# Optimization experiments

Hardware: AMD Instinct MI355X
Metric: run time of the kernel (lower is better)

## Reference

```python
import jax, jax.numpy as jnp
import numpy as np

D = 256      # input channels
DK = 64      # key/query/value channels
BS, W, H = 8, 64, 64


def setup_inputs() -> dict:
    key = jax.random.key(0)
    k1, k2, k3, k4 = jax.random.split(key, 4)
    v = jax.random.normal(k1, (BS, D, W, H), dtype=jnp.float32)
    # conv1x1 weights collapse to plain matrices over the channel dim
    Wqkv = jax.random.normal(k2, (3 * DK, D), dtype=jnp.float32) * 0.02
    Wout = jax.random.normal(k3, (D, DK), dtype=jnp.float32) * 0.02
    gamma = jax.random.normal(k4, (1,), dtype=jnp.float32)  # original inits to 0; nonzero for a non-degenerate baseline
    return {"v": v, "Wqkv": Wqkv, "Wout": Wout, "gamma": gamma}


def reference(v, Wqkv, Wout, gamma):
    bs, c, w, h = v.shape
    n = w * h
    d_k = Wout.shape[1]
    x = v.reshape(bs, c, n)                      # (b, c, n)
    qkv = jnp.einsum('oc,bcn->bon', Wqkv, x)      # 1x1 conv == channel matmul
    q = qkv[:, :d_k]                              # (b, dk, n)
    k = qkv[:, d_k:2 * d_k]
    val = qkv[:, 2 * d_k:]
    s = jnp.einsum('bdi,bdj->bij', q, k)          # (b, n, n) = query^T key
    beta = jax.nn.softmax(s, axis=2)              # exp(s - logsumexp(s, axis=2))
    y = jnp.einsum('bdi,bij->bdj', val, beta)     # bmm(value, beta)
    o = jnp.einsum('od,bdn->bon', Wout, y) * gamma[0] + x
    return o.reshape(bs, c, w, h)
```

## Files before the change

### kernel.cpp

```cpp
#include <hip/hip_runtime.h>

typedef unsigned short ushort_t;
typedef __bf16 bf16x8 __attribute__((ext_vector_type(8)));
typedef short short4v __attribute__((ext_vector_type(4)));
typedef float f32x4 __attribute__((ext_vector_type(4)));
typedef unsigned int uint4v __attribute__((ext_vector_type(4)));
typedef unsigned int uint2v __attribute__((ext_vector_type(2)));

#define NTOK 4096
#define DMODEL 256
#define DK 64
#define BS 8
#define LN2INV 1.44269504088896f

__device__ __forceinline__ ushort_t f2bf(float f) {
  unsigned u = __builtin_bit_cast(unsigned, f);
  u += 0x7fffu + ((u >> 16) & 1u);
  return (ushort_t)(u >> 16);
}
__device__ __forceinline__ float bf2f(ushort_t s) {
  return __builtin_bit_cast(float, ((unsigned)s) << 16);
}
__device__ __forceinline__ bf16x8 lds_frag(const ushort_t* p) {
  return __builtin_bit_cast(bf16x8, *(const uint4v*)p);
}
__device__ __forceinline__ float fexp2(float x) {
#if __has_builtin(__builtin_amdgcn_exp2f)
  return __builtin_amdgcn_exp2f(x);
#else
  return exp2f(x);
#endif
}
__device__ __forceinline__ unsigned bfpack(float x, float y) {
  return __builtin_amdgcn_perm(__builtin_bit_cast(unsigned, y),
                               __builtin_bit_cast(unsigned, x), 0x07060302u);
}
__device__ __forceinline__ f32x4 mfma16(short4v a, short4v b, f32x4 c) {
#if defined(__HIP_DEVICE_COMPILE__)
#if __has_builtin(__builtin_amdgcn_mfma_f32_16x16x16bf16_1k)
  return __builtin_amdgcn_mfma_f32_16x16x16bf16_1k(a, b, c, 0, 0, 0);
#else
  typedef __bf16 bf16x4 __attribute__((ext_vector_type(4)));
  return __builtin_amdgcn_mfma_f32_16x16x16_bf16(__builtin_bit_cast(bf16x4, a),
                                                 __builtin_bit_cast(bf16x4, b), c, 0, 0, 0);
#endif
#else
  (void)a; (void)b;
  return c;
#endif
}

__global__ __launch_bounds__(256) void k_convert(const float* __restrict__ Wqkv,
                                                 const float* __restrict__ Wout,
                                                 ushort_t* __restrict__ Wb,
                                                 ushort_t* __restrict__ Woutb) {
  int i = blockIdx.x * 256 + threadIdx.x;
  if (i < 3 * DK * DMODEL) {
    float w = Wqkv[i];
    if (i < DK * DMODEL) w *= LN2INV;
    Wb[i] = f2bf(w);
  } else {
    int j = i - 3 * DK * DMODEL;
    Woutb[j] = f2bf(Wout[j]);
  }
}

__global__ __launch_bounds__(256) void k_transpose(const float* __restrict__ x,
                                                   ushort_t* __restrict__ xT) {
  const int id = blockIdx.x;
  const int b = id & 7;
  const int rest = id >> 3;
  const int c0 = (rest & 3) * 64;
  const int n0 = (rest >> 2) * 64;
  const int tid = threadIdx.x;
  __shared__ __align__(16) ushort_t t[64 * 72];
  const float* xb = x + (size_t)b * DMODEL * NTOK;
  ushort_t* xTb = xT + (size_t)b * NTOK * DMODEL;
#pragma unroll
  for (int kr = 0; kr < 2; kr++) {
    int s = tid + 256 * kr;
    int c = s >> 3, ns = (s & 7) * 8;
    const float* src = xb + (size_t)(c0 + c) * NTOK + n0 + ns;
    f32x4 a = *(const f32x4*)src;
    f32x4 bq = *(const f32x4*)(src + 4);
    uint4v o;
    o.x = (unsigned)f2bf(a[0]) | ((unsigned)f2bf(a[1]) << 16);
    o.y = (unsigned)f2bf(a[2]) | ((unsigned)f2bf(a[3]) << 16);
    o.z = (unsigned)f2bf(bq[0]) | ((unsigned)f2bf(bq[1]) << 16);
    o.w = (unsigned)f2bf(bq[2]) | ((unsigned)f2bf(bq[3]) << 16);
    *(uint4v*)(t + c * 72 + ns) = o;
  }
  __syncthreads();
#pragma unroll
  for (int kr = 0; kr < 2; kr++) {
    int s = tid + 256 * kr;
    int n = s >> 3, cs = (s & 7) * 8;
    unsigned e0 = t[(cs + 0) * 72 + n], e1 = t[(cs + 1) * 72 + n];
    unsigned e2 = t[(cs + 2) * 72 + n], e3 = t[(cs + 3) * 72 + n];
    unsigned e4 = t[(cs + 4) * 72 + n], e5 = t[(cs + 5) * 72 + n];
    unsigned e6 = t[(cs + 6) * 72 + n], e7 = t[(cs + 7) * 72 + n];
    uint4v o;
    o.x = e0 | (e1 << 16); o.y = e2 | (e3 << 16);
    o.z = e4 | (e5 << 16); o.w = e6 | (e7 << 16);
    *(uint4v*)(xTb + (size_t)(n0 + n) * DMODEL + c0 + cs) = o;
  }
}

__global__ __launch_bounds__(256) void k_qkv(const ushort_t* __restrict__ xT,
                                             const ushort_t* __restrict__ W,
                                             ushort_t* __restrict__ QT,
                                             ushort_t* __restrict__ KT,
                                             ushort_t* __restrict__ Vv) {
  const int id = blockIdx.x;
  const int b = id & 7;
  const int n0 = (id >> 3) * 64;
  const int tid = threadIdx.x;
  const int lane = tid & 63, wv = tid >> 6;
  const int quad = lane >> 4, l15 = lane & 15;
  __shared__ __align__(16) ushort_t lw[192 * 40];
  __shared__ __align__(16) ushort_t lx[64 * 40];
  f32x4 acc[3][4];
  const f32x4 zero4 = {0.f, 0.f, 0.f, 0.f};
#pragma unroll
  for (int i = 0; i < 3; i++)
#pragma unroll
    for (int j = 0; j < 4; j++) acc[i][j] = zero4;

  const ushort_t* xTb = xT + ((size_t)b * NTOK + n0) * DMODEL;

  for (int c0 = 0; c0 < DMODEL; c0 += 32) {
    __syncthreads();
#pragma unroll
    for (int kr = 0; kr < 3; kr++) {
      int s = tid + 256 * kr;
      int o = s >> 2, cs = (s & 3) * 8;
      *(uint4v*)(lw + o * 40 + cs) = *(const uint4v*)(W + o * DMODEL + c0 + cs);
    }
    {
      int n = tid >> 2, cs = (tid & 3) * 8;
      *(uint4v*)(lx + n * 40 + cs) = *(const uint4v*)(xTb + (size_t)n * DMODEL + c0 + cs);
    }
    __syncthreads();
    bf16x8 bb[4];
#pragma unroll
    for (int nt = 0; nt < 4; nt++) bb[nt] = lds_frag(lx + (nt * 16 + l15) * 40 + quad * 8);
#pragma unroll
    for (int mt = 0; mt < 3; mt++) {
      bf16x8 a = lds_frag(lw + (wv * 48 + mt * 16 + l15) * 40 + quad * 8);
#pragma unroll
      for (int nt = 0; nt < 4; nt++)
        acc[mt][nt] = __builtin_amdgcn_mfma_f32_16x16x32_bf16(a, bb[nt], acc[mt][nt], 0, 0, 0);
    }
  }
#pragma unroll
  for (int mt = 0; mt < 3; mt++) {
    int o = wv * 48 + mt * 16 + quad * 4;
#pragma unroll
    for (int nt = 0; nt < 4; nt++) {
      int n = n0 + nt * 16 + l15;
      f32x4 v4 = acc[mt][nt];
      if (o < 128) {
        ushort_t* dst = (o < 64) ? (QT + ((size_t)b * NTOK + n) * DK + o)
                                 : (KT + ((size_t)b * NTOK + n) * DK + (o - 64));
        uint2v ww;
        ww.x = (unsigned)f2bf(v4[0]) | ((unsigned)f2bf(v4[1]) << 16);
        ww.y = (unsigned)f2bf(v4[2]) | ((unsigned)f2bf(v4[3]) << 16);
        *(uint2v*)dst = ww;
      } else {
        int d = o - 128;
#pragma unroll
        for (int r = 0; r < 4; r++)
          Vv[((size_t)b * DK + d + r) * NTOK + n] = f2bf(v4[r]);
      }
    }
  }
}

__global__ __launch_bounds__(256) void k_rsum(const ushort_t* __restrict__ QT,
                                              const ushort_t* __restrict__ KT,
                                              float* __restrict__ Rp) {
  const int id = blockIdx.x;
  const int b = id & 7;
  const int rest = id >> 3;
  const int i0 = (rest & 31) * 128;
  const int jh = rest >> 5;
  const int tid = threadIdx.x;
  const int lane = tid & 63, wv = tid >> 6;
  const int quad = lane >> 4, l15 = lane & 15;
  __shared__ __align__(16) ushort_t lq[128 * 72];
  __shared__ __align__(16) ushort_t lk[2][64 * 72];
  const ushort_t* QTb = QT + ((size_t)b * NTOK + i0) * DK;
  const ushort_t* KTb = KT + ((size_t)b * NTOK + jh * 2048) * DK;
#pragma unroll
  for (int kr = 0; kr < 4; kr++) {
    int s = tid + 256 * kr;
    int row = s >> 3, ds = (s & 7) * 8;
    *(uint4v*)(lq + row * 72 + ds) = *(const uint4v*)(QTb + (size_t)row * DK + ds);
  }
#pragma unroll
  for (int kr = 0; kr < 2; kr++) {
    int s = tid + 256 * kr;
    int row = s >> 3, ds = (s & 7) * 8;
    *(uint4v*)(lk[0] + row * 72 + ds) = *(const uint4v*)(KTb + (size_t)row * DK + ds);
  }
  __syncthreads();
  bf16x8 aa[2][2];
#pragma unroll
  for (int isub = 0; isub < 2; isub++) {
    aa[isub][0] = lds_frag(lq + (wv * 32 + isub * 16 + l15) * 72 + quad * 8);
    aa[isub][1] = lds_frag(lq + (wv * 32 + isub * 16 + l15) * 72 + 32 + quad * 8);
  }
  float lsum[2][4];
#pragma unroll
  for (int i = 0; i < 2; i++)
#pragma unroll
    for (int r = 0; r < 4; r++) lsum[i][r] = 0.f;
  const f32x4 zero4 = {0.f, 0.f, 0.f, 0.f};

  auto stage = [&](ushort_t* dstb, int itn) {
    const ushort_t* src = KTb + (size_t)itn * 64 * DK;
#pragma unroll
    for (int kr = 0; kr < 2; kr++) {
      int s = tid + 256 * kr;
      int row = s >> 3, ds = (s & 7) * 8;
      *(uint4v*)(dstb + row * 72 + ds) = *(const uint4v*)(src + (size_t)row * DK + ds);
    }
  };
  auto body = [&](const ushort_t* kb) {
#pragma unroll
    for (int nt = 0; nt < 4; nt++) {
      bf16x8 b0 = lds_frag(kb + (nt * 16 + l15) * 72 + quad * 8);
      bf16x8 b1 = lds_frag(kb + (nt * 16 + l15) * 72 + 32 + quad * 8);
#pragma unroll
      for (int isub = 0; isub < 2; isub++) {
        f32x4 s4 = __builtin_amdgcn_mfma_f32_16x16x32_bf16(aa[isub][0], b0, zero4, 0, 0, 0);
        s4 = __builtin_amdgcn_mfma_f32_16x16x32_bf16(aa[isub][1], b1, s4, 0, 0, 0);
        lsum[isub][0] += fexp2(s4[0]);
        lsum[isub][1] += fexp2(s4[1]);
        lsum[isub][2] += fexp2(s4[2]);
        lsum[isub][3] += fexp2(s4[3]);
      }
    }
  };

  for (int it2 = 0; it2 < 16; it2++) {
    int it = it2 * 2;
    stage(lk[1], it + 1);
    body(lk[0]);
    __syncthreads();
    if (it2 < 15) stage(lk[0], it + 2);
    body(lk[1]);
    __syncthreads();
  }

#pragma unroll
  for (int isub = 0; isub < 2; isub++)
#pragma unroll
    for (int r = 0; r < 4; r++)
#pragma unroll
      for (int off = 1; off < 16; off <<= 1) lsum[isub][r] += __shfl_xor(lsum[isub][r], off);
  if (l15 < 8) {
    int rr = l15 & 3, isub = l15 >> 2;
    float va = (rr == 0) ? lsum[0][0] : (rr == 1) ? lsum[0][1] : (rr == 2) ? lsum[0][2] : lsum[0][3];
    float vb = (rr == 0) ? lsum[1][0] : (rr == 1) ? lsum[1][1] : (rr == 2) ? lsum[1][2] : lsum[1][3];
    float v = isub ? vb : va;
    Rp[((size_t)(jh * 8 + b)) * NTOK + i0 + wv * 32 + isub * 16 + quad * 4 + rr] = v;
  }
}

__global__ __launch_bounds__(256) void k_rv(const float* __restrict__ Rp,
                                            ushort_t* __restrict__ Vv) {
  const int id = blockIdx.x;
  const int b = id & 7;
  const int ibase = (id >> 3) * 256;
  const int tid = threadIdx.x;
  __shared__ float lrr[256];
  size_t g = (size_t)b * NTOK + ibase + tid;
  lrr[tid] = 1.0f / (Rp[g] + Rp[(size_t)8 * NTOK + g]);
  __syncthreads();
  const int dsub = tid >> 5;
  const int ioff = (tid & 31) * 8;
#pragma unroll
  for (int d8 = 0; d8 < 8; d8++) {
    int d = d8 * 8 + dsub;
    ushort_t* vp = Vv + ((size_t)b * DK + d) * NTOK + ibase + ioff;
    uint4v v0 = *(const uint4v*)vp;
    uint4v o0;
    unsigned* vi = (unsigned*)&v0;
    unsigned* oo = (unsigned*)&o0;
#pragma unroll
    for (int w = 0; w < 4; w++) {
      float e0 = bf2f((ushort_t)(vi[w] & 0xffff)) * lrr[ioff + 2 * w];
      float e1 = bf2f((ushort_t)(vi[w] >> 16)) * lrr[ioff + 2 * w + 1];
      oo[w] = (unsigned)f2bf(e0) | ((unsigned)f2bf(e1) << 16);
    }
    *(uint4v*)vp = o0;
  }
}

__global__ __launch_bounds__(256) void k_pv(const ushort_t* __restrict__ QT,
                                            const ushort_t* __restrict__ KT,
                                            const ushort_t* __restrict__ Vv,
                                            ushort_t* __restrict__ Yp) {
  const int id = blockIdx.x;
  const int b = id & 7;
  const int rest = id >> 3;
  const int j0 = (rest & 63) * 64;
  const int ih = rest >> 6;
  const int tid = threadIdx.x;
  const int lane = tid & 63, wv = tid >> 6;
  const int quad = lane >> 4, l15 = lane & 15;

  __shared__ __align__(16) ushort_t pool[18432];
#define LQ(buf) (pool + (buf) * 4608)
#define LV(buf) (pool + 9216 + (buf) * 4608)
  float* rbuf = (float*)pool;
  ushort_t* pbuf = pool + 8704;

  const ushort_t* KTb = KT + ((size_t)b * NTOK + j0) * DK;
  const ushort_t* QTb = QT + ((size_t)b * NTOK + ih * 2048) * DK;
  const ushort_t* Vbb = Vv + (size_t)b * DK * NTOK + ih * 2048;

#pragma unroll
  for (int kr = 0; kr < 2; kr++) {
    int s = tid + 256 * kr;
    int row = s >> 3, ds = (s & 7) * 8;
    *(uint4v*)(LQ(0) + row * 72 + ds) = *(const uint4v*)(KTb + (size_t)row * DK + ds);
  }
  __syncthreads();
  bf16x8 kb0[4], kb1[4];
#pragma unroll
  for (int nt = 0; nt < 4; nt++) {
    kb0[nt] = lds_frag(LQ(0) + (nt * 16 + l15) * 72 + quad * 8);
    kb1[nt] = lds_frag(LQ(0) + (nt * 16 + l15) * 72 + 32 + quad * 8);
  }
  __syncthreads();
#pragma unroll
  for (int kr = 0; kr < 2; kr++) {
    int s = tid + 256 * kr;
    int row = s >> 3, ds = (s & 7) * 8;
    *(uint4v*)(LQ(0) + row * 72 + ds) = *(const uint4v*)(QTb + (size_t)row * DK + ds);
    *(uint4v*)(LV(0) + row * 72 + ds) = *(const uint4v*)(Vbb + (size_t)row * NTOK + ds);
  }
  __syncthreads();

  const f32x4 zero4 = {0.f, 0.f, 0.f, 0.f};
  f32x4 yt[4][4];
#pragma unroll
  for (int i = 0; i < 4; i++)
#pragma unroll
    for (int j = 0; j < 4; j++) yt[i][j] = zero4;

  auto stage = [&](ushort_t* lqn, ushort_t* lvn, int itn) {
    const ushort_t* qsrc = QTb + (size_t)itn * 64 * DK;
    const ushort_t* vsrc = Vbb + itn * 64;
#pragma unroll
    for (int kr = 0; kr < 2; kr++) {
      int s = tid + 256 * kr;
      int row = s >> 3, ds = (s & 7) * 8;
      *(uint4v*)(lqn + row * 72 + ds) = *(const uint4v*)(qsrc + (size_t)row * DK + ds);
      *(uint4v*)(lvn + row * 72 + ds) = *(const uint4v*)(vsrc + (size_t)row * NTOK + ds);
    }
  };
  auto body = [&](const ushort_t* lqc, const ushort_t* lvc) {
    bf16x8 a0 = lds_frag(lqc + (wv * 16 + l15) * 72 + quad * 8);
    bf16x8 a1 = lds_frag(lqc + (wv * 16 + l15) * 72 + 32 + quad * 8);
    short4v vf[4];
#pragma unroll
    for (int dsub = 0; dsub < 4; dsub++)
      vf[dsub] = __builtin_bit_cast(short4v,
          *(const uint2v*)(lvc + (dsub * 16 + l15) * 72 + wv * 16 + quad * 4));
#pragma unroll
    for (int nt = 0; nt < 4; nt++) {
      f32x4 s4 = __builtin_amdgcn_mfma_f32_16x16x32_bf16(a0, kb0[nt], zero4, 0, 0, 0);
      s4 = __builtin_amdgcn_mfma_f32_16x16x32_bf16(a1, kb1[nt], s4, 0, 0, 0);
      uint2v wp;
      wp.x = bfpack(fexp2(s4[0]), fexp2(s4[1]));
      wp.y = bfpack(fexp2(s4[2]), fexp2(s4[3]));
      short4v wf = __builtin_bit_cast(short4v, wp);
#pragma unroll
      for (int dsub = 0; dsub < 4; dsub++)
        yt[nt][dsub] = mfma16(wf, vf[dsub], yt[nt][dsub]);
    }
  };

  for (int it2 = 0; it2 < 16; it2++) {
    int it = it2 * 2;
    stage(LQ(1), LV(1), it + 1);
    body(LQ(0), LV(0));
    __syncthreads();
    if (it2 < 15) stage(LQ(0), LV(0), it + 2);
    body(LQ(1), LV(1));
    __syncthreads();
  }

  if (wv == 0) {
#pragma unroll
    for (int nt = 0; nt < 4; nt++)
#pragma unroll
      for (int dsub = 0; dsub < 4; dsub++)
        *(f32x4*)(rbuf + (dsub * 16 + l15) * 68 + nt * 16 + quad * 4) = yt[nt][dsub];
  }
  __syncthreads();
  if (wv == 1) {
#pragma unroll
    for (int nt = 0; nt < 4; nt++)
#pragma unroll
      for (int dsub = 0; dsub < 4; dsub++) {
        float* p = rbuf + (dsub * 16 + l15) * 68 + nt * 16 + quad * 4;
        *(f32x4*)p = *(const f32x4*)p + yt[nt][dsub];
      }
  }
  __syncthreads();
  if (wv == 2) {
#pragma unroll
    for (int nt = 0; nt < 4; nt++)
#pragma unroll
      for (int dsub = 0; dsub < 4; dsub++) {
        float* p = rbuf + (dsub * 16 + l15) * 68 + nt * 16 + quad * 4;
        *(f32x4*)p = *(const f32x4*)p + yt[nt][dsub];
      }
  }
  __syncthreads();
  if (wv == 3) {
#pragma unroll
    for (int nt = 0; nt < 4; nt++)
#pragma unroll
      for (int dsub = 0; dsub < 4; dsub++) {
        const float* p = rbuf + (dsub * 16 + l15) * 68 + nt * 16 + quad * 4;
        f32x4 v4 = *(const f32x4*)p + yt[nt][dsub];
#pragma unroll
        for (int r = 0; r < 4; r++)
          pbuf[(nt * 16 + quad * 4 + r) * 72 + dsub * 16 + l15] = f2bf(v4[r]);
      }
  }
  __syncthreads();

  ushort_t* Ypb = Yp + ((size_t)(ih * 8 + b) * NTOK + j0) * DK;
#pragma unroll
  for (int kr = 0; kr < 2; kr++) {
    int s = tid + 256 * kr;
    int row = s >> 3, c8 = (s & 7) * 8;
    *(uint4v*)(Ypb + (size_t)row * DK + c8) = *(const uint4v*)(pbuf + row * 72 + c8);
  }
#undef LQ
#undef LV
}

__global__ __launch_bounds__(256) void k_out(const ushort_t* __restrict__ Yp,
                                             const ushort_t* __restrict__ Wout,
                                             const float* __restrict__ gammap,
                                             const float* __restrict__ x,
                                             float* __restrict__ outp) {
  const int id = blockIdx.x;
  const int b = id & 7;
  const int n0 = (id >> 3) * 64;
  const int tid = threadIdx.x;
  const int lane = tid & 63, wv = tid >> 6;
  const int quad = lane >> 4, l15 = lane & 15;
  __shared__ __align__(16) ushort_t pbuf[64 * 72];

  const ushort_t* Y0 = Yp + ((size_t)b * NTOK + n0) * DK;
  const ushort_t* Y1 = Yp + ((size_t)(8 + b) * NTOK + n0) * DK;
#pragma unroll
  for (int kr = 0; kr < 2; kr++) {
    int s = tid + 256 * kr;
    int row = s >> 3, c8 = (s & 7) * 8;
    uint4v ua = *(const uint4v*)(Y0 + (size_t)row * DK + c8);
    uint4v ub = *(const uint4v*)(Y1 + (size_t)row * DK + c8);
    uint4v oc;
    unsigned* pa = (unsigned*)&ua;
    unsigned* pb = (unsigned*)&ub;
    unsigned* po = (unsigned*)&oc;
#pragma unroll
    for (int w = 0; w < 4; w++) {
      float lo = bf2f((ushort_t)(pa[w] & 0xffff)) + bf2f((ushort_t)(pb[w] & 0xffff));
      float hi = bf2f((ushort_t)(pa[w] >> 16)) + bf2f((ushort_t)(pb[w] >> 16));
      po[w] = bfpack(lo, hi);
    }
    *(uint4v*)(pbuf + row * 72 + c8) = oc;
  }
  __syncthreads();

  const f32x4 zero4 = {0.f, 0.f, 0.f, 0.f};
  bf16x8 yb0[4], yb1[4];
#pragma unroll
  for (int nt = 0; nt < 4; nt++) {
    yb0[nt] = lds_frag(pbuf + (nt * 16 + l15) * 72 + quad * 8);
    yb1[nt] = lds_frag(pbuf + (nt * 16 + l15) * 72 + 32 + quad * 8);
  }
  f32x4 oacc[4][4];
#pragma unroll
  for (int m = 0; m < 4; m++)
#pragma unroll
    for (int nt = 0; nt < 4; nt++) oacc[m][nt] = zero4;
#pragma unroll
  for (int m = 0; m < 4; m++) {
    int c = (wv * 4 + m) * 16 + l15;
    bf16x8 aw0 = __builtin_bit_cast(bf16x8, *(const uint4v*)(Wout + c * DK + quad * 8));
    bf16x8 aw1 = __builtin_bit_cast(bf16x8, *(const uint4v*)(Wout + c * DK + 32 + quad * 8));
#pragma unroll
    for (int nt = 0; nt < 4; nt++) {
      oacc[m][nt] = __builtin_amdgcn_mfma_f32_16x16x32_bf16(aw0, yb0[nt], oacc[m][nt], 0, 0, 0);
      oacc[m][nt] = __builtin_amdgcn_mfma_f32_16x16x32_bf16(aw1, yb1[nt], oacc[m][nt], 0, 0, 0);
    }
  }
  float g = gammap[0];
  const float* xb = x + (size_t)b * DMODEL * NTOK;
  float* ob = outp + (size_t)b * DMODEL * NTOK;
#pragma unroll
  for (int m = 0; m < 4; m++) {
    int cbase = (wv * 4 + m) * 16 + quad * 4;
#pragma unroll
    for (int nt = 0; nt < 4; nt++) {
      int n = n0 + nt * 16 + l15;
#pragma unroll
      for (int r = 0; r < 4; r++) {
        size_t idx = (size_t)(cbase + r) * NTOK + n;
        ob[idx] = oacc[m][nt][r] * g + xb[idx];
      }
    }
  }
}

extern "C" void kernel_launch(void* const* d_in, const int* in_sizes, int n_in,
                              void* d_out, int out_size, void* d_ws, size_t ws_size,
                              hipStream_t stream) {
  const float* v = (const float*)d_in[0];
  const float* Wqkv = (const float*)d_in[1];
  const float* Wout = (const float*)d_in[2];
  const float* gamma = (const float*)d_in[3];
  float* outp = (float*)d_out;

  ushort_t* xT = (ushort_t*)d_ws;
  ushort_t* QT = xT + (size_t)BS * NTOK * DMODEL;
  ushort_t* KT = QT + (size_t)BS * NTOK * DK;
  ushort_t* Vs = KT + (size_t)BS * NTOK * DK;
  ushort_t* Wb = Vs + (size_t)BS * DK * NTOK;
  ushort_t* Woutb = Wb + 3 * DK * DMODEL;
  float* Rp = (float*)(Woutb + DMODEL * DK);
  ushort_t* Yp = (ushort_t*)(Rp + 2 * (size_t)BS * NTOK);

  k_convert<<<dim3(256), 256, 0, stream>>>(Wqkv, Wout, Wb, Woutb);
  k_transpose<<<dim3(2048), 256, 0, stream>>>(v, xT);
  k_qkv<<<dim3(512), 256, 0, stream>>>(xT, Wb, QT, KT, Vs);
  k_rsum<<<dim3(512), 256, 0, stream>>>(QT, KT, Rp);
  k_rv<<<dim3(128), 256, 0, stream>>>(Rp, Vs);
  k_pv<<<dim3(1024), 256, 0, stream>>>(QT, KT, Vs, Yp);
  k_out<<<dim3(512), 256, 0, stream>>>(Yp, Woutb, gamma, v, outp);
}
```

Before: 228.1 us.

## Load Q/V fragments directly from global in k_pv; halve k_rsum row tile

In k_pv the double-buffered LDS staging of Q and V tiles and its per-iteration barriers are removed; each lane now loads its MFMA fragments straight from global memory, and the LDS pool shrinks. k_rsum uses 64-row query tiles instead of 128, doubling the grid to 1024 blocks with a simpler single-subtile accumulation. The aim is to cut LDS traffic and barrier stalls and raise occupancy. The cost is uncoalesced, latency-exposed global loads in the inner loop, plus twice as many K tile reloads in k_rsum.

```diff
diff --git a/kernel.cpp b/kernel.cpp
--- a/kernel.cpp
+++ b/kernel.cpp
@@ -21,7 +21,7 @@
 __device__ __forceinline__ float bf2f(ushort_t s) {
   return __builtin_bit_cast(float, ((unsigned)s) << 16);
 }
-__device__ __forceinline__ bf16x8 lds_frag(const ushort_t* p) {
+__device__ __forceinline__ bf16x8 ld_frag(const ushort_t* p) {
   return __builtin_bit_cast(bf16x8, *(const uint4v*)p);
 }
 __device__ __forceinline__ float fexp2(float x) {
@@ -143,10 +143,10 @@
     __syncthreads();
     bf16x8 bb[4];
 #pragma unroll
-    for (int nt = 0; nt < 4; nt++) bb[nt] = lds_frag(lx + (nt * 16 + l15) * 40 + quad * 8);
+    for (int nt = 0; nt < 4; nt++) bb[nt] = ld_frag(lx + (nt * 16 + l15) * 40 + quad * 8);
 #pragma unroll
     for (int mt = 0; mt < 3; mt++) {
-      bf16x8 a = lds_frag(lw + (wv * 48 + mt * 16 + l15) * 40 + quad * 8);
+      bf16x8 a = ld_frag(lw + (wv * 48 + mt * 16 + l15) * 40 + quad * 8);
 #pragma unroll
       for (int nt = 0; nt < 4; nt++)
         acc[mt][nt] = __builtin_amdgcn_mfma_f32_16x16x32_bf16(a, bb[nt], acc[mt][nt], 0, 0, 0);
@@ -182,39 +182,26 @@
   const int id = blockIdx.x;
   const int b = id & 7;
   const int rest = id >> 3;
-  const int i0 = (rest & 31) * 128;
-  const int jh = rest >> 5;
+  const int i0 = (rest & 63) * 64;
+  const int jh = rest >> 6;
   const int tid = threadIdx.x;
   const int lane = tid & 63, wv = tid >> 6;
   const int quad = lane >> 4, l15 = lane & 15;
-  __shared__ __align__(16) ushort_t lq[128 * 72];
+  __shared__ __align__(16) ushort_t lq[64 * 72];
   __shared__ __align__(16) ushort_t lk[2][64 * 72];
   const ushort_t* QTb = QT + ((size_t)b * NTOK + i0) * DK;
   const ushort_t* KTb = KT + ((size_t)b * NTOK + jh * 2048) * DK;
 #pragma unroll
-  for (int kr = 0; kr < 4; kr++) {
+  for (int kr = 0; kr < 2; kr++) {
     int s = tid + 256 * kr;
     int row = s >> 3, ds = (s & 7) * 8;
     *(uint4v*)(lq + row * 72 + ds) = *(const uint4v*)(QTb + (size_t)row * DK + ds);
-  }
-#pragma unroll
-  for (int kr = 0; kr < 2; kr++) {
-    int s = tid + 256 * kr;
-    int row = s >> 3, ds = (s & 7) * 8;
     *(uint4v*)(lk[0] + row * 72 + ds) = *(const uint4v*)(KTb + (size_t)row * DK + ds);
   }
   __syncthreads();
-  bf16x8 aa[2][2];
-#pragma unroll
-  for (int isub = 0; isub < 2; isub++) {
-    aa[isub][0] = lds_frag(lq + (wv * 32 + isub * 16 + l15) * 72 + quad * 8);
-    aa[isub][1] = lds_frag(lq + (wv * 32 + isub * 16 + l15) * 72 + 32 + quad * 8);
-  }
-  float lsum[2][4];
-#pragma unroll
-  for (int i = 0; i < 2; i++)
-#pragma unroll
-    for (int r = 0; r < 4; r++) lsum[i][r] = 0.f;
+  bf16x8 a0 = ld_frag(lq + (wv * 16 + l15) * 72 + quad * 8);
+  bf16x8 a1 = ld_frag(lq + (wv * 16 + l15) * 72 + 32 + quad * 8);
+  float lsum0 = 0.f, lsum1 = 0.f, lsum2 = 0.f, lsum3 = 0.f;
   const f32x4 zero4 = {0.f, 0.f, 0.f, 0.f};
 
   auto stage = [&](ushort_t* dstb, int itn) {
@@ -229,17 +216,14 @@
   auto body = [&](const ushort_t* kb) {
 #pragma unroll
     for (int nt = 0; nt < 4; nt++) {
-      bf16x8 b0 = lds_frag(kb + (nt * 16 + l15) * 72 + quad * 8);
-      bf16x8 b1 = lds_frag(kb + (nt * 16 + l15) * 72 + 32 + quad * 8);
-#pragma unroll
-      for (int isub = 0; isub < 2; isub++) {
-        f32x4 s4 = __builtin_amdgcn_mfma_f32_16x16x32_bf16(aa[isub][0], b0, zero4, 0, 0, 0);
-        s4 = __builtin_amdgcn_mfma_f32_16x16x32_bf16(aa[isub][1], b1, s4, 0, 0, 0);
-        lsum[isub][0] += fexp2(s4[0]);
-        lsum[isub][1] += fexp2(s4[1]);
-        lsum[isub][2] += fexp2(s4[2]);
-        lsum[isub][3] += fexp2(s4[3]);
-      }
+      bf16x8 b0 = ld_frag(kb + (nt * 16 + l15) * 72 + quad * 8);
+      bf16x8 b1 = ld_frag(kb + (nt * 16 + l15) * 72 + 32 + quad * 8);
+      f32x4 s4 = __builtin_amdgcn_mfma_f32_16x16x32_bf16(a0, b0, zero4, 0, 0, 0);
+      s4 = __builtin_amdgcn_mfma_f32_16x16x32_bf16(a1, b1, s4, 0, 0, 0);
+      lsum0 += fexp2(s4[0]);
+      lsum1 += fexp2(s4[1]);
+      lsum2 += fexp2(s4[2]);
+      lsum3 += fexp2(s4[3]);
     }
   };
 
@@ -254,17 +238,15 @@
   }
 
 #pragma unroll
-  for (int isub = 0; isub < 2; isub++)
-#pragma unroll
-    for (int r = 0; r < 4; r++)
-#pragma unroll
-      for (int off = 1; off < 16; off <<= 1) lsum[isub][r] += __shfl_xor(lsum[isub][r], off);
-  if (l15 < 8) {
-    int rr = l15 & 3, isub = l15 >> 2;
-    float va = (rr == 0) ? lsum[0][0] : (rr == 1) ? lsum[0][1] : (rr == 2) ? lsum[0][2] : lsum[0][3];
-    float vb = (rr == 0) ? lsum[1][0] : (rr == 1) ? lsum[1][1] : (rr == 2) ? lsum[1][2] : lsum[1][3];
-    float v = isub ? vb : va;
-    Rp[((size_t)(jh * 8 + b)) * NTOK + i0 + wv * 32 + isub * 16 + quad * 4 + rr] = v;
+  for (int off = 1; off < 16; off <<= 1) {
+    lsum0 += __shfl_xor(lsum0, off);
+    lsum1 += __shfl_xor(lsum1, off);
+    lsum2 += __shfl_xor(lsum2, off);
+    lsum3 += __shfl_xor(lsum3, off);
+  }
+  if (l15 < 4) {
+    float v = (l15 == 0) ? lsum0 : (l15 == 1) ? lsum1 : (l15 == 2) ? lsum2 : lsum3;
+    Rp[((size_t)(jh * 8 + b)) * NTOK + i0 + wv * 16 + quad * 4 + l15] = v;
   }
 }
 
@@ -311,9 +293,7 @@
   const int lane = tid & 63, wv = tid >> 6;
   const int quad = lane >> 4, l15 = lane & 15;
 
-  __shared__ __align__(16) ushort_t pool[18432];
-#define LQ(buf) (pool + (buf) * 4608)
-#define LV(buf) (pool + 9216 + (buf) * 4608)
+  __shared__ __align__(16) ushort_t pool[13312];
   float* rbuf = (float*)pool;
   ushort_t* pbuf = pool + 8704;
 
@@ -325,22 +305,14 @@
   for (int kr = 0; kr < 2; kr++) {
     int s = tid + 256 * kr;
     int row = s >> 3, ds = (s & 7) * 8;
-    *(uint4v*)(LQ(0) + row * 72 + ds) = *(const uint4v*)(KTb + (size_t)row * DK + ds);
+    *(uint4v*)(pool + row * 72 + ds) = *(const uint4v*)(KTb + (size_t)row * DK + ds);
   }
   __syncthreads();
   bf16x8 kb0[4], kb1[4];
 #pragma unroll
   for (int nt = 0; nt < 4; nt++) {
-    kb0[nt] = lds_frag(LQ(0) + (nt * 16 + l15) * 72 + quad * 8);
-    kb1[nt] = lds_frag(LQ(0) + (nt * 16 + l15) * 72 + 32 + quad * 8);
-  }
-  __syncthreads();
-#pragma unroll
-  for (int kr = 0; kr < 2; kr++) {
-    int s = tid + 256 * kr;
-    int row = s >> 3, ds = (s & 7) * 8;
-    *(uint4v*)(LQ(0) + row * 72 + ds) = *(const uint4v*)(QTb + (size_t)row * DK + ds);
-    *(uint4v*)(LV(0) + row * 72 + ds) = *(const uint4v*)(Vbb + (size_t)row * NTOK + ds);
+    kb0[nt] = ld_frag(pool + (nt * 16 + l15) * 72 + quad * 8);
+    kb1[nt] = ld_frag(pool + (nt * 16 + l15) * 72 + 32 + quad * 8);
   }
   __syncthreads();
 
@@ -351,25 +323,19 @@
 #pragma unroll
     for (int j = 0; j < 4; j++) yt[i][j] = zero4;
 
-  auto stage = [&](ushort_t* lqn, ushort_t* lvn, int itn) {
-    const ushort_t* qsrc = QTb + (size_t)itn * 64 * DK;
-    const ushort_t* vsrc = Vbb + itn * 64;
-#pragma unroll
-    for (int kr = 0; kr < 2; kr++) {
-      int s = tid + 256 * kr;
-      int row = s >> 3, ds = (s & 7) * 8;
-      *(uint4v*)(lqn + row * 72 + ds) = *(const uint4v*)(qsrc + (size_t)row * DK + ds);
-      *(uint4v*)(lvn + row * 72 + ds) = *(const uint4v*)(vsrc + (size_t)row * NTOK + ds);
-    }
-  };
-  auto body = [&](const ushort_t* lqc, const ushort_t* lvc) {
-    bf16x8 a0 = lds_frag(lqc + (wv * 16 + l15) * 72 + quad * 8);
-    bf16x8 a1 = lds_frag(lqc + (wv * 16 + l15) * 72 + 32 + quad * 8);
+  const ushort_t* qlane = QTb + (size_t)(wv * 16 + l15) * DK + quad * 8;
+  const ushort_t* vlane = Vbb + (size_t)l15 * NTOK + wv * 16 + quad * 4;
+
+#pragma unroll 2
+  for (int it = 0; it < 32; it++) {
+    const ushort_t* qit = qlane + (size_t)it * 64 * DK;
+    bf16x8 a0 = ld_frag(qit);
+    bf16x8 a1 = ld_frag(qit + 32);
+    const ushort_t* vit = vlane + it * 64;
     short4v vf[4];
 #pragma unroll
     for (int dsub = 0; dsub < 4; dsub++)
-      vf[dsub] = __builtin_bit_cast(short4v,
-          *(const uint2v*)(lvc + (dsub * 16 + l15) * 72 + wv * 16 + quad * 4));
+      vf[dsub] = __builtin_bit_cast(short4v, *(const uint2v*)(vit + (size_t)dsub * 16 * NTOK));
 #pragma unroll
     for (int nt = 0; nt < 4; nt++) {
       f32x4 s4 = __builtin_amdgcn_mfma_f32_16x16x32_bf16(a0, kb0[nt], zero4, 0, 0, 0);
@@ -382,16 +348,6 @@
       for (int dsub = 0; dsub < 4; dsub++)
         yt[nt][dsub] = mfma16(wf, vf[dsub], yt[nt][dsub]);
     }
-  };
-
-  for (int it2 = 0; it2 < 16; it2++) {
-    int it = it2 * 2;
-    stage(LQ(1), LV(1), it + 1);
-    body(LQ(0), LV(0));
-    __syncthreads();
-    if (it2 < 15) stage(LQ(0), LV(0), it + 2);
-    body(LQ(1), LV(1));
-    __syncthreads();
   }
 
   if (wv == 0) {
@@ -443,8 +399,6 @@
     int row = s >> 3, c8 = (s & 7) * 8;
     *(uint4v*)(Ypb + (size_t)row * DK + c8) = *(const uint4v*)(pbuf + row * 72 + c8);
   }
-#undef LQ
-#undef LV
 }
 
 __global__ __launch_bounds__(256) void k_out(const ushort_t* __restrict__ Yp,
@@ -486,8 +440,8 @@
   bf16x8 yb0[4], yb1[4];
 #pragma unroll
   for (int nt = 0; nt < 4; nt++) {
-    yb0[nt] = lds_frag(pbuf + (nt * 16 + l15) * 72 + quad * 8);
-    yb1[nt] = lds_frag(pbuf + (nt * 16 + l15) * 72 + 32 + quad * 8);
+    yb0[nt] = ld_frag(pbuf + (nt * 16 + l15) * 72 + quad * 8);
+    yb1[nt] = ld_frag(pbuf + (nt * 16 + l15) * 72 + 32 + quad * 8);
   }
   f32x4 oacc[4][4];
 #pragma unroll
@@ -544,7 +498,7 @@
   k_convert<<<dim3(256), 256, 0, stream>>>(Wqkv, Wout, Wb, Woutb);
   k_transpose<<<dim3(2048), 256, 0, stream>>>(v, xT);
   k_qkv<<<dim3(512), 256, 0, stream>>>(xT, Wb, QT, KT, Vs);
-  k_rsum<<<dim3(512), 256, 0, stream>>>(QT, KT, Rp);
+  k_rsum<<<dim3(1024), 256, 0, stream>>>(QT, KT, Rp);
   k_rv<<<dim3(128), 256, 0, stream>>>(Rp, Vs);
   k_pv<<<dim3(1024), 256, 0, stream>>>(QT, KT, Vs, Yp);
   k_out<<<dim3(512), 256, 0, stream>>>(Yp, Woutb, gamma, v, outp);
```

After: 252.6 us. +10.7%, slower.
